# Optimization experiments

Hardware: AMD Instinct MI355X
Metric: run time of the kernel (lower is better)

Reference implementation:

```python
import jax, jax.numpy as jnp
import numpy as np

B, S, D, H = 2, 2048, 1024, 16
DK = D // H


def setup_inputs() -> dict:
    key = jax.random.key(0)
    ks = jax.random.split(key, 12)
    sc = 0.02
    inp = {
        "q": jax.random.normal(ks[0], (B, S, D), jnp.float32),
        "k": jax.random.normal(ks[1], (B, S, D), jnp.float32),
        "v": jax.random.normal(ks[2], (B, S, D), jnp.float32),
        "mask": jnp.ones((B, S, S), jnp.int32),
        "Wq": jax.random.normal(ks[3], (D, D), jnp.float32) * sc,
        "bq": jnp.zeros((D,), jnp.float32),
        "Wk": jax.random.normal(ks[4], (D, D), jnp.float32) * sc,
        "bk": jnp.zeros((D,), jnp.float32),
        "Wv": jax.random.normal(ks[5], (D, D), jnp.float32) * sc,
        "bv": jnp.zeros((D,), jnp.float32),
        "Wo": jax.random.normal(ks[6], (D, D), jnp.float32) * sc,
        "bo": jnp.zeros((D,), jnp.float32),
    }
    return inp


def _split_heads(x):
    # [B,S,D] -> [B,H,S,DK]
    b, s, _ = x.shape
    return x.reshape(b, s, H, DK).transpose(0, 2, 1, 3)


def reference(q, k, v, mask, Wq, bq, Wk, bk, Wv, bv, Wo, bo):
    qh = _split_heads(q @ Wq.T + bq)
    kh = _split_heads(k @ Wk.T + bk)
    vh = _split_heads(v @ Wv.T + bv)
    scale = 1.0 / jnp.sqrt(jnp.float32(DK))
    scores = jnp.einsum("bhqd,bhkd->bhqk", qh, kh) * scale  # [B,H,S,S]
    scores = jnp.where(mask[:, None, :, :] == 0, jnp.float32(-1e9), scores)
    probs = jax.nn.softmax(scores, axis=-1)  # dropout p=0.0 -> identity
    out = jnp.einsum("bhqk,bhkd->bhqd", probs, vh)  # [B,H,S,DK]
    concat = out.transpose(0, 2, 1, 3).reshape(q.shape[0], -1, D)
    return concat @ Wo.T + bo
```

## Files before the change

kernel.cpp:

```cpp
#include <hip/hip_runtime.h>
#include <stdint.h>

#define Bsz 2
#define Ssz 2048
#define Dsz 1024
#define Hsz 16
#define DKsz 64

typedef __attribute__((ext_vector_type(8))) short sh8;
typedef __attribute__((ext_vector_type(4))) float fx4;
typedef __attribute__((ext_vector_type(16))) float fx16;
typedef __attribute__((ext_vector_type(4))) unsigned ux4;

__device__ __forceinline__ unsigned short f2bf(float x) {
  uint32_t u = __builtin_bit_cast(uint32_t, x);
  uint32_t r = (u + 0x7fffu + ((u >> 16) & 1u)) >> 16;
  return (unsigned short)r;
}

__device__ __forceinline__ fx4 mfma16(sh8 a, sh8 b, fx4 c) {
  return __builtin_amdgcn_mfma_f32_16x16x32_bf16(a, b, c, 0, 0, 0);
}

__device__ __forceinline__ fx16 mfma32(sh8 a, sh8 b, fx16 c) {
  return __builtin_amdgcn_mfma_f32_32x32x16_bf16(a, b, c, 0, 0, 0);
}

__device__ __forceinline__ void g2l16(const void* g, void* l) {
  __builtin_amdgcn_global_load_lds((const __attribute__((address_space(1))) void*)g,
                                   (__attribute__((address_space(3))) void*)l, 16, 0, 0);
}

__device__ __forceinline__ float fexp2(float x) {
#if __has_builtin(__builtin_amdgcn_exp2f)
  return __builtin_amdgcn_exp2f(x);
#else
  return exp2f(x);
#endif
}

__device__ __forceinline__ unsigned cvtpk(float lo, float hi) {
  unsigned r;
  asm("v_cvt_pk_bf16_f32 %0, %1, %2" : "=v"(r) : "v"(lo), "v"(hi));
  return r;
}

__device__ __forceinline__ void plswap(unsigned& a, unsigned& b) {
  asm("v_permlane32_swap_b32 %0, %1" : "+v"(a), "+v"(b));
}

__device__ __forceinline__ void build_pa(const fx16& p, sh8& pa0, sh8& pa1) {
  unsigned w0 = cvtpk(p[0], p[1]), w1 = cvtpk(p[2], p[3]);
  unsigned w2 = cvtpk(p[4], p[5]), w3 = cvtpk(p[6], p[7]);
  unsigned w4 = cvtpk(p[8], p[9]), w5 = cvtpk(p[10], p[11]);
  unsigned w6 = cvtpk(p[12], p[13]), w7 = cvtpk(p[14], p[15]);
  plswap(w0, w2);
  plswap(w1, w3);
  ux4 u0 = {w0, w1, w2, w3};
  pa0 = __builtin_bit_cast(sh8, u0);
  plswap(w4, w6);
  plswap(w5, w7);
  ux4 u1 = {w4, w5, w6, w7};
  pa1 = __builtin_bit_cast(sh8, u1);
}

__global__ __launch_bounds__(256) void convert_kernel(
    const float* __restrict__ q, const float* __restrict__ k, const float* __restrict__ v,
    const float* __restrict__ wq, const float* __restrict__ wk, const float* __restrict__ wv,
    const float* __restrict__ wo,
    unsigned short* __restrict__ qb, unsigned short* __restrict__ kb, unsigned short* __restrict__ vb,
    unsigned short* __restrict__ wqb, unsigned short* __restrict__ wkb, unsigned short* __restrict__ wvb,
    unsigned short* __restrict__ wob) {
  const int NQ = Bsz * Ssz * Dsz / 4;
  const int NW = Dsz * Dsz / 4;
  const int total = 3 * NQ + 4 * NW;
  for (int i = blockIdx.x * blockDim.x + threadIdx.x; i < total; i += gridDim.x * blockDim.x) {
    const float* src; unsigned short* dst; int off;
    if (i < 3 * NQ) {
      int t = i / NQ; off = i - t * NQ;
      src = (t == 0) ? q : ((t == 1) ? k : v);
      dst = (t == 0) ? qb : ((t == 1) ? kb : vb);
    } else {
      int j = i - 3 * NQ; int t = j / NW; off = j - t * NW;
      src = (t == 0) ? wq : ((t == 1) ? wk : ((t == 2) ? wv : wo));
      dst = (t == 0) ? wqb : ((t == 1) ? wkb : ((t == 2) ? wvb : wob));
    }
    float4 x = ((const float4*)src)[off];
    ushort4 o;
    o.x = f2bf(x.x); o.y = f2bf(x.y); o.z = f2bf(x.z); o.w = f2bf(x.w);
    ((ushort4*)dst)[off] = o;
  }
}

__global__ void flag_init_kernel(int* flag) {
  if (threadIdx.x == 0 && blockIdx.x == 0) flag[0] = 1;
}

__global__ __launch_bounds__(256) void mask_check_kernel(const int* __restrict__ mask,
                                                         int* __restrict__ flag) {
  const int n4 = Bsz * Ssz * Ssz / 4;
  int bad = 0;
  for (int i = blockIdx.x * blockDim.x + threadIdx.x; i < n4; i += gridDim.x * blockDim.x) {
    int4 m = ((const int4*)mask)[i];
    if (m.x == 0 || m.y == 0 || m.z == 0 || m.w == 0) bad = 1;
  }
  if (bad) atomicAnd(flag, 0);
}

__global__ __launch_bounds__(256) void proj_qkv_kernel(
    const unsigned short* __restrict__ qb, const unsigned short* __restrict__ kb,
    const unsigned short* __restrict__ vb,
    const unsigned short* __restrict__ wqb, const unsigned short* __restrict__ wkb,
    const unsigned short* __restrict__ wvb,
    const float* __restrict__ bq, const float* __restrict__ bk, const float* __restrict__ bv,
    unsigned short* __restrict__ qh, unsigned short* __restrict__ kh,
    unsigned short* __restrict__ vt) {
  __shared__ __align__(16) unsigned short As[128 * 32];
  __shared__ __align__(16) unsigned short Bs[128 * 32];
  __shared__ __align__(16) unsigned short Ts[128 * 136];
  const int z = blockIdx.z;
  const unsigned short* X = (z == 0) ? qb : ((z == 1) ? kb : vb);
  const unsigned short* W = (z == 0) ? wqb : ((z == 1) ? wkb : wvb);
  const float* bias = (z == 0) ? bq : ((z == 1) ? bk : bv);
  const int m0 = blockIdx.x * 128, n0 = blockIdx.y * 128;
  const int tid = threadIdx.x, lane = tid & 63, wid = tid >> 6;
  const int wm = wid >> 1, wn = wid & 1;
  const int c = lane & 15, g = lane >> 4;
  fx4 acc[4][4] = {};
  for (int k0 = 0; k0 < Dsz; k0 += 32) {
#pragma unroll
    for (int i = 0; i < 2; i++) {
      int e = i * 256 + tid;
      g2l16(X + (size_t)(m0 + (e >> 2)) * Dsz + k0 + (e & 3) * 8,
            (char*)As + (size_t)(i * 256 + wid * 64) * 16);
      g2l16(W + (size_t)(n0 + (e >> 2)) * Dsz + k0 + (e & 3) * 8,
            (char*)Bs + (size_t)(i * 256 + wid * 64) * 16);
    }
    __syncthreads();
    sh8 af[4], bfr[4];
#pragma unroll
    for (int m = 0; m < 4; m++)
      af[m] = *(const sh8*)&As[(wm * 64 + m * 16 + c) * 32 + g * 8];
#pragma unroll
    for (int n = 0; n < 4; n++)
      bfr[n] = *(const sh8*)&Bs[(wn * 64 + n * 16 + c) * 32 + g * 8];
#pragma unroll
    for (int m = 0; m < 4; m++)
#pragma unroll
      for (int n = 0; n < 4; n++)
        acc[m][n] = mfma16(af[m], bfr[n], acc[m][n]);
    __syncthreads();
  }
  if (z < 2) {
    unsigned short* O = (z == 0) ? qh : kh;
#pragma unroll
    for (int n = 0; n < 4; n++) {
      int j = n0 + wn * 64 + n * 16 + c;
      float bj = bias[j];
      int h = j >> 6, dk = j & 63;
#pragma unroll
      for (int m = 0; m < 4; m++)
#pragma unroll
        for (int r = 0; r < 4; r++) {
          int i = m0 + wm * 64 + m * 16 + g * 4 + r;
          int b = i >> 11, s = i & 2047;
          O[(((size_t)(b * Hsz + h) * Ssz + s) << 6) + dk] = f2bf(acc[m][n][r] + bj);
        }
    }
  } else {
#pragma unroll
    for (int n = 0; n < 4; n++) {
      int nl = wn * 64 + n * 16 + c;
      float bj = bias[n0 + nl];
#pragma unroll
      for (int m = 0; m < 4; m++)
#pragma unroll
        for (int r = 0; r < 4; r++) {
          int ml = wm * 64 + m * 16 + g * 4 + r;
          Ts[nl * 136 + ml] = f2bf(acc[m][n][r] + bj);
        }
    }
    __syncthreads();
    int b = m0 >> 11, sbase = m0 & 2047;
#pragma unroll
    for (int it = 0; it < 8; it++) {
      int ch = it * 256 + tid;
      int row = ch >> 4, off = ch & 15;
      sh8 dv = *(const sh8*)&Ts[row * 136 + off * 8];
      int j = n0 + row;
      int h = j >> 6, dk = j & 63;
      *(sh8*)&vt[(size_t)((b * Hsz + h) * DKsz + dk) * Ssz + sbase + off * 8] = dv;
    }
  }
}

__global__ __launch_bounds__(256) void attn_kernel(
    const unsigned short* __restrict__ qh, const unsigned short* __restrict__ kh,
    const unsigned short* __restrict__ vt, const int* __restrict__ mask,
    const int* __restrict__ flag, unsigned short* __restrict__ concat) {
  __shared__ __align__(16) unsigned short Ks[2][64 * 64];
  __shared__ __align__(16) unsigned short Vs[2][64 * 64];
  const int tid = threadIdx.x, lane = tid & 63, wid = tid >> 6;
  const int bh = blockIdx.y, b = bh >> 4, h = bh & 15;
  const int q0 = blockIdx.x * 128 + wid * 32;
  const int c = lane & 31, hi = lane >> 5;
  const int cs = c & 7;
  const unsigned short* Qb = qh + ((size_t)bh * Ssz + q0) * DKsz;
  const unsigned short* Kb = kh + (size_t)bh * Ssz * DKsz;
  const unsigned short* Vb = vt + (size_t)bh * DKsz * Ssz;
  const int ch0 = wid * 128 + lane;
  const int ch1 = ch0 + 64;
  const int r0 = ch0 >> 3, sl0 = (ch0 & 7) ^ (r0 & 7);
  const int r1 = ch1 >> 3, sl1 = (ch1 & 7) ^ (r1 & 7);
  const int koff0 = r0 * DKsz + sl0 * 8, koff1 = r1 * DKsz + sl1 * 8;
  const size_t voff0 = (size_t)r0 * Ssz + sl0 * 8, voff1 = (size_t)r1 * Ssz + sl1 * 8;

  sh8 qf[4];
#pragma unroll
  for (int ks = 0; ks < 4; ks++)
    qf[ks] = *(const sh8*)&Qb[(size_t)c * DKsz + ks * 16 + hi * 8];
  const bool allones = (flag[0] != 0);
  const float CE = 0.18033688011112042f;
  float mrun = -1e30f, lsum = 0.f;
  fx16 o0 = {}, o1 = {};

  auto STAGE = [&](int bufi, int kv0) {
    const unsigned short* ksrc = Kb + (size_t)kv0 * DKsz;
    g2l16(ksrc + koff0, (char*)&Ks[bufi][0] + (size_t)wid * 2048);
    g2l16(ksrc + koff1, (char*)&Ks[bufi][0] + (size_t)wid * 2048 + 1024);
    const unsigned short* vsrc = Vb + kv0;
    g2l16(vsrc + voff0, (char*)&Vs[bufi][0] + (size_t)wid * 2048);
    g2l16(vsrc + voff1, (char*)&Vs[bufi][0] + (size_t)wid * 2048 + 1024);
  };

  STAGE(0, 0);
  asm volatile("s_waitcnt vmcnt(0)" ::: "memory");
  __builtin_amdgcn_s_barrier();
  asm volatile("" ::: "memory");

  const int NT = Ssz / 64;
  for (int t = 0; t < NT; ++t) {
    const int cur = t & 1;
    const int kv0 = t * 64;
    if (t + 1 < NT) STAGE(cur ^ 1, kv0 + 64);
    fx16 s0 = {}, s1 = {};
#pragma unroll
    for (int ks = 0; ks < 4; ks++) {
      int sl = (2 * ks + hi) ^ cs;
      sh8 ka = *(const sh8*)&Ks[cur][(c * 8 + sl) * 8];
      sh8 kb2 = *(const sh8*)&Ks[cur][((32 + c) * 8 + sl) * 8];
      s0 = mfma32(ka, qf[ks], s0);
      s1 = mfma32(kb2, qf[ks], s1);
    }
    if (!allones) {
      const int* mrow = mask + ((size_t)b * Ssz + (q0 + c)) * Ssz + kv0;
#pragma unroll
      for (int r = 0; r < 16; r++) {
        int kv = (r & 3) + 8 * (r >> 2) + 4 * hi;
        if (mrow[kv] == 0) s0[r] = -1e9f;
        if (mrow[32 + kv] == 0) s1[r] = -1e9f;
      }
    }
    float mx = fmaxf(s0[0], s0[1]);
#pragma unroll
    for (int r = 2; r < 16; r++) mx = fmaxf(mx, s0[r]);
#pragma unroll
    for (int r = 0; r < 16; r++) mx = fmaxf(mx, s1[r]);
    mx = fmaxf(mx, __shfl_xor(mx, 32));
    float mn = fmaxf(mrun, mx);
    float fr = fexp2(CE * (mrun - mn));
    mrun = mn;
    float mc = mn * CE;
#pragma unroll
    for (int r = 0; r < 16; r++) {
      s0[r] = fexp2(__builtin_fmaf(s0[r], CE, -mc));
      s1[r] = fexp2(__builtin_fmaf(s1[r], CE, -mc));
    }
    float ps = 0.f;
#pragma unroll
    for (int r = 0; r < 16; r++) ps += s0[r] + s1[r];
    lsum = lsum * fr + ps;
#pragma unroll
    for (int r = 0; r < 16; r++) { o0[r] *= fr; o1[r] *= fr; }
    sh8 pa[4];
    build_pa(s0, pa[0], pa[1]);
    build_pa(s1, pa[2], pa[3]);
#pragma unroll
    for (int ks = 0; ks < 4; ks++) {
      int sl = (2 * ks + hi) ^ cs;
      sh8 v0f = *(const sh8*)&Vs[cur][(c * 8 + sl) * 8];
      sh8 v1f = *(const sh8*)&Vs[cur][((32 + c) * 8 + sl) * 8];
      o0 = mfma32(v0f, pa[ks], o0);
      o1 = mfma32(v1f, pa[ks], o1);
    }
    asm volatile("s_waitcnt vmcnt(0)" ::: "memory");
    __builtin_amdgcn_s_barrier();
    asm volatile("" ::: "memory");
  }
  lsum += __shfl_xor(lsum, 32);
  float linv = 1.0f / lsum;
  unsigned short* Ob = concat + ((size_t)b * Ssz + q0 + c) * Dsz + h * DKsz;
#pragma unroll
  for (int rg = 0; rg < 4; rg++) {
    ushort4 w;
    w.x = f2bf(o0[rg * 4 + 0] * linv);
    w.y = f2bf(o0[rg * 4 + 1] * linv);
    w.z = f2bf(o0[rg * 4 + 2] * linv);
    w.w = f2bf(o0[rg * 4 + 3] * linv);
    *(ushort4*)&Ob[8 * rg + 4 * hi] = w;
    ushort4 w2;
    w2.x = f2bf(o1[rg * 4 + 0] * linv);
    w2.y = f2bf(o1[rg * 4 + 1] * linv);
    w2.z = f2bf(o1[rg * 4 + 2] * linv);
    w2.w = f2bf(o1[rg * 4 + 3] * linv);
    *(ushort4*)&Ob[32 + 8 * rg + 4 * hi] = w2;
  }
}

__global__ __launch_bounds__(256) void outproj_kernel(
    const unsigned short* __restrict__ Xc, const unsigned short* __restrict__ wob,
    const float* __restrict__ bo, float* __restrict__ out) {
  __shared__ __align__(16) unsigned short As[128 * 32];
  __shared__ __align__(16) unsigned short Bs[128 * 32];
  const int m0 = blockIdx.x * 128, n0 = blockIdx.y * 128;
  const int tid = threadIdx.x, lane = tid & 63, wid = tid >> 6;
  const int wm = wid >> 1, wn = wid & 1;
  const int c = lane & 15, g = lane >> 4;
  fx4 acc[4][4] = {};
  for (int k0 = 0; k0 < Dsz; k0 += 32) {
#pragma unroll
    for (int i = 0; i < 2; i++) {
      int e = i * 256 + tid;
      g2l16(Xc + (size_t)(m0 + (e >> 2)) * Dsz + k0 + (e & 3) * 8,
            (char*)As + (size_t)(i * 256 + wid * 64) * 16);
      g2l16(wob + (size_t)(n0 + (e >> 2)) * Dsz + k0 + (e & 3) * 8,
            (char*)Bs + (size_t)(i * 256 + wid * 64) * 16);
    }
    __syncthreads();
    sh8 af[4], bfr[4];
#pragma unroll
    for (int m = 0; m < 4; m++)
      af[m] = *(const sh8*)&As[(wm * 64 + m * 16 + c) * 32 + g * 8];
#pragma unroll
    for (int n = 0; n < 4; n++)
      bfr[n] = *(const sh8*)&Bs[(wn * 64 + n * 16 + c) * 32 + g * 8];
#pragma unroll
    for (int m = 0; m < 4; m++)
#pragma unroll
      for (int n = 0; n < 4; n++)
        acc[m][n] = mfma16(af[m], bfr[n], acc[m][n]);
    __syncthreads();
  }
#pragma unroll
  for (int n = 0; n < 4; n++) {
    int j = n0 + wn * 64 + n * 16 + c;
    float bj = bo[j];
#pragma unroll
    for (int m = 0; m < 4; m++)
#pragma unroll
      for (int r = 0; r < 4; r++) {
        int i = m0 + wm * 64 + m * 16 + g * 4 + r;
        out[(size_t)i * Dsz + j] = acc[m][n][r] + bj;
      }
  }
}

extern "C" void kernel_launch(void* const* d_in, const int* in_sizes, int n_in,
                              void* d_out, int out_size, void* d_ws, size_t ws_size,
                              hipStream_t stream) {
  const float* q = (const float*)d_in[0];
  const float* k = (const float*)d_in[1];
  const float* v = (const float*)d_in[2];
  const int* mask = (const int*)d_in[3];
  const float* Wq = (const float*)d_in[4];
  const float* bq = (const float*)d_in[5];
  const float* Wk = (const float*)d_in[6];
  const float* bk = (const float*)d_in[7];
  const float* Wv = (const float*)d_in[8];
  const float* bv = (const float*)d_in[9];
  const float* Wo = (const float*)d_in[10];
  const float* bo = (const float*)d_in[11];
  float* out = (float*)d_out;
  char* ws = (char*)d_ws;
  const size_t MB = 1 << 20;
  unsigned short* qb  = (unsigned short*)(ws + 0 * MB);
  unsigned short* kb  = (unsigned short*)(ws + 8 * MB);
  unsigned short* vb  = (unsigned short*)(ws + 16 * MB);
  unsigned short* wqb = (unsigned short*)(ws + 24 * MB);
  unsigned short* wkb = (unsigned short*)(ws + 26 * MB);
  unsigned short* wvb = (unsigned short*)(ws + 28 * MB);
  unsigned short* wob = (unsigned short*)(ws + 30 * MB);
  unsigned short* qhp = (unsigned short*)(ws + 32 * MB);
  unsigned short* khp = (unsigned short*)(ws + 40 * MB);
  unsigned short* vtp = (unsigned short*)(ws + 48 * MB);
  unsigned short* cc  = (unsigned short*)(ws + 56 * MB);
  int* flag = (int*)(ws + 64 * MB);

  hipLaunchKernelGGL(flag_init_kernel, dim3(1), dim3(64), 0, stream, flag);
  hipLaunchKernelGGL(mask_check_kernel, dim3(2048), dim3(256), 0, stream, mask, flag);
  hipLaunchKernelGGL(convert_kernel, dim3(2048), dim3(256), 0, stream,
                     q, k, v, Wq, Wk, Wv, Wo, qb, kb, vb, wqb, wkb, wvb, wob);
  hipLaunchKernelGGL(proj_qkv_kernel, dim3(32, 8, 3), dim3(256), 0, stream,
                     qb, kb, vb, wqb, wkb, wvb, bq, bk, bv, qhp, khp, vtp);
  hipLaunchKernelGGL(attn_kernel, dim3(16, 32), dim3(256), 0, stream,
                     qhp, khp, vtp, mask, flag, cc);
  hipLaunchKernelGGL(outproj_kernel, dim3(32, 8), dim3(256), 0, stream,
                     cc, wob, bo, out);
}
```

Measured before the change: 160.6 us.

## Triple-buffer attention K/V, lazy softmax rescale, fold mask check into convert

Several changes at once. The attention kernel moves from double to triple buffering of K/V tiles with two tiles in flight, and raises wave priority around the MFMA blocks. The online softmax becomes lazy: exponentials use the stale running max, and the accumulators are rescaled only when the new max exceeds it by a threshold, which takes the max reduction off the critical path. The mask scan also merges into the convert kernel to save a launch. The risks are more LDS per block and possible overflow if the threshold logic misjudges the spread of the scores.

```diff
diff --git a/kernel.cpp b/kernel.cpp
--- a/kernel.cpp
+++ b/kernel.cpp
@@ -67,14 +67,22 @@
 __global__ __launch_bounds__(256) void convert_kernel(
     const float* __restrict__ q, const float* __restrict__ k, const float* __restrict__ v,
     const float* __restrict__ wq, const float* __restrict__ wk, const float* __restrict__ wv,
-    const float* __restrict__ wo,
+    const float* __restrict__ wo, const int* __restrict__ mask,
     unsigned short* __restrict__ qb, unsigned short* __restrict__ kb, unsigned short* __restrict__ vb,
     unsigned short* __restrict__ wqb, unsigned short* __restrict__ wkb, unsigned short* __restrict__ wvb,
-    unsigned short* __restrict__ wob) {
+    unsigned short* __restrict__ wob, int* __restrict__ flag) {
   const int NQ = Bsz * Ssz * Dsz / 4;
   const int NW = Dsz * Dsz / 4;
-  const int total = 3 * NQ + 4 * NW;
+  const int NC = 3 * NQ + 4 * NW;
+  const int NM = Bsz * Ssz * Ssz / 4;
+  const int total = NC + NM;
+  int bad = 0;
   for (int i = blockIdx.x * blockDim.x + threadIdx.x; i < total; i += gridDim.x * blockDim.x) {
+    if (i >= NC) {
+      int4 m = ((const int4*)mask)[i - NC];
+      if (m.x == 0 || m.y == 0 || m.z == 0 || m.w == 0) bad = 1;
+      continue;
+    }
     const float* src; unsigned short* dst; int off;
     if (i < 3 * NQ) {
       int t = i / NQ; off = i - t * NQ;
@@ -90,21 +98,11 @@
     o.x = f2bf(x.x); o.y = f2bf(x.y); o.z = f2bf(x.z); o.w = f2bf(x.w);
     ((ushort4*)dst)[off] = o;
   }
+  if (bad) atomicAnd(flag, 0);
 }
 
 __global__ void flag_init_kernel(int* flag) {
   if (threadIdx.x == 0 && blockIdx.x == 0) flag[0] = 1;
-}
-
-__global__ __launch_bounds__(256) void mask_check_kernel(const int* __restrict__ mask,
-                                                         int* __restrict__ flag) {
-  const int n4 = Bsz * Ssz * Ssz / 4;
-  int bad = 0;
-  for (int i = blockIdx.x * blockDim.x + threadIdx.x; i < n4; i += gridDim.x * blockDim.x) {
-    int4 m = ((const int4*)mask)[i];
-    if (m.x == 0 || m.y == 0 || m.z == 0 || m.w == 0) bad = 1;
-  }
-  if (bad) atomicAnd(flag, 0);
 }
 
 __global__ __launch_bounds__(256) void proj_qkv_kernel(
@@ -198,8 +196,8 @@
     const unsigned short* __restrict__ qh, const unsigned short* __restrict__ kh,
     const unsigned short* __restrict__ vt, const int* __restrict__ mask,
     const int* __restrict__ flag, unsigned short* __restrict__ concat) {
-  __shared__ __align__(16) unsigned short Ks[2][64 * 64];
-  __shared__ __align__(16) unsigned short Vs[2][64 * 64];
+  __shared__ __align__(16) unsigned short Ks[3][64 * 64];
+  __shared__ __align__(16) unsigned short Vs[3][64 * 64];
   const int tid = threadIdx.x, lane = tid & 63, wid = tid >> 6;
   const int bh = blockIdx.y, b = bh >> 4, h = bh & 15;
   const int q0 = blockIdx.x * 128 + wid * 32;
@@ -221,7 +219,8 @@
     qf[ks] = *(const sh8*)&Qb[(size_t)c * DKsz + ks * 16 + hi * 8];
   const bool allones = (flag[0] != 0);
   const float CE = 0.18033688011112042f;
-  float mrun = -1e30f, lsum = 0.f;
+  const float THRraw = 8.0f / CE;
+  float mrun = 0.0f, lsum = 0.f;
   fx16 o0 = {}, o1 = {};
 
   auto STAGE = [&](int bufi, int kv0) {
@@ -233,17 +232,20 @@
     g2l16(vsrc + voff1, (char*)&Vs[bufi][0] + (size_t)wid * 2048 + 1024);
   };
 
+  const int NT = Ssz / 64;
   STAGE(0, 0);
-  asm volatile("s_waitcnt vmcnt(0)" ::: "memory");
+  STAGE(1, 64);
+  asm volatile("s_waitcnt vmcnt(4)" ::: "memory");
   __builtin_amdgcn_s_barrier();
   asm volatile("" ::: "memory");
 
-  const int NT = Ssz / 64;
+  int cur = 0;
   for (int t = 0; t < NT; ++t) {
-    const int cur = t & 1;
     const int kv0 = t * 64;
-    if (t + 1 < NT) STAGE(cur ^ 1, kv0 + 64);
+    int nxt2 = cur + 2; if (nxt2 >= 3) nxt2 -= 3;
+    if (t + 2 < NT) STAGE(nxt2, kv0 + 128);
     fx16 s0 = {}, s1 = {};
+    __builtin_amdgcn_s_setprio(1);
 #pragma unroll
     for (int ks = 0; ks < 4; ks++) {
       int sl = (2 * ks + hi) ^ cs;
@@ -252,6 +254,7 @@
       s0 = mfma32(ka, qf[ks], s0);
       s1 = mfma32(kb2, qf[ks], s1);
     }
+    __builtin_amdgcn_s_setprio(0);
     if (!allones) {
       const int* mrow = mask + ((size_t)b * Ssz + (q0 + c)) * Ssz + kv0;
 #pragma unroll
@@ -261,30 +264,17 @@
         if (mrow[32 + kv] == 0) s1[r] = -1e9f;
       }
     }
-    float mx = fmaxf(s0[0], s0[1]);
-#pragma unroll
-    for (int r = 2; r < 16; r++) mx = fmaxf(mx, s0[r]);
-#pragma unroll
-    for (int r = 0; r < 16; r++) mx = fmaxf(mx, s1[r]);
-    mx = fmaxf(mx, __shfl_xor(mx, 32));
-    float mn = fmaxf(mrun, mx);
-    float fr = fexp2(CE * (mrun - mn));
-    mrun = mn;
-    float mc = mn * CE;
+    const float mc = mrun * CE;
+    fx16 p0v, p1v;
 #pragma unroll
     for (int r = 0; r < 16; r++) {
-      s0[r] = fexp2(__builtin_fmaf(s0[r], CE, -mc));
-      s1[r] = fexp2(__builtin_fmaf(s1[r], CE, -mc));
-    }
-    float ps = 0.f;
-#pragma unroll
-    for (int r = 0; r < 16; r++) ps += s0[r] + s1[r];
-    lsum = lsum * fr + ps;
-#pragma unroll
-    for (int r = 0; r < 16; r++) { o0[r] *= fr; o1[r] *= fr; }
+      p0v[r] = fexp2(__builtin_fmaf(s0[r], CE, -mc));
+      p1v[r] = fexp2(__builtin_fmaf(s1[r], CE, -mc));
+    }
     sh8 pa[4];
-    build_pa(s0, pa[0], pa[1]);
-    build_pa(s1, pa[2], pa[3]);
+    build_pa(p0v, pa[0], pa[1]);
+    build_pa(p1v, pa[2], pa[3]);
+    __builtin_amdgcn_s_setprio(1);
 #pragma unroll
     for (int ks = 0; ks < 4; ks++) {
       int sl = (2 * ks + hi) ^ cs;
@@ -293,9 +283,37 @@
       o0 = mfma32(v0f, pa[ks], o0);
       o1 = mfma32(v1f, pa[ks], o1);
     }
-    asm volatile("s_waitcnt vmcnt(0)" ::: "memory");
+    __builtin_amdgcn_s_setprio(0);
+    float sm[16], mxv[16];
+#pragma unroll
+    for (int r = 0; r < 16; r++) {
+      sm[r] = p0v[r] + p1v[r];
+      mxv[r] = fmaxf(s0[r], s1[r]);
+    }
+#pragma unroll
+    for (int w = 8; w >= 1; w >>= 1)
+#pragma unroll
+      for (int r = 0; r < w; r++) {
+        sm[r] += sm[r + w];
+        mxv[r] = fmaxf(mxv[r], mxv[r + w]);
+      }
+    lsum += sm[0];
+    float mx = fmaxf(mxv[0], __shfl_xor(mxv[0], 32));
+    if (__any(mx > mrun + THRraw)) {
+      float mnew = fmaxf(mrun, mx);
+      float fr = fexp2(CE * (mrun - mnew));
+      lsum *= fr;
+#pragma unroll
+      for (int r = 0; r < 16; r++) { o0[r] *= fr; o1[r] *= fr; }
+      mrun = mnew;
+    }
+    if (t < NT - 2)
+      asm volatile("s_waitcnt vmcnt(4)" ::: "memory");
+    else
+      asm volatile("s_waitcnt vmcnt(0)" ::: "memory");
     __builtin_amdgcn_s_barrier();
     asm volatile("" ::: "memory");
+    cur++; if (cur >= 3) cur = 0;
   }
   lsum += __shfl_xor(lsum, 32);
   float linv = 1.0f / lsum;
@@ -397,9 +415,8 @@
   int* flag = (int*)(ws + 64 * MB);
 
   hipLaunchKernelGGL(flag_init_kernel, dim3(1), dim3(64), 0, stream, flag);
-  hipLaunchKernelGGL(mask_check_kernel, dim3(2048), dim3(256), 0, stream, mask, flag);
   hipLaunchKernelGGL(convert_kernel, dim3(2048), dim3(256), 0, stream,
-                     q, k, v, Wq, Wk, Wv, Wo, qb, kb, vb, wqb, wkb, wvb, wob);
+                     q, k, v, Wq, Wk, Wv, Wo, mask, qb, kb, vb, wqb, wkb, wvb, wob, flag);
   hipLaunchKernelGGL(proj_qkv_kernel, dim3(32, 8, 3), dim3(256), 0, stream,
                      qb, kb, vb, wqb, wkb, wvb, bq, bk, bv, qhp, khp, vtp);
   hipLaunchKernelGGL(attn_kernel, dim3(16, 32), dim3(256), 0, stream,
```

After: 155.4 us. -3.3%, faster.
